# Performance work log

Hardware: AMD Instinct MI355X
Metric: run time of the kernel (lower is better)

The kernel has to match this reference:

```python
import jax, jax.numpy as jnp
import numpy as np

B, S, E, H = 2, 2048, 1024, 16
DH = E // H            # 64 head dim
ROT = DH // 2          # 32: RotaryEmbedding(head_dim//2) rotates first 32 dims only
CTX = 2048             # sliding KV window
THETA = 10000.0


def setup_inputs() -> dict:
    key = jax.random.key(0)
    ks = jax.random.split(key, 7)
    sc = 1.0 / np.sqrt(E)
    mk = lambda k, sh, s=1.0: (jax.random.normal(k, sh, jnp.float32) * s)
    return {
        "query": mk(ks[0], (B, S, E)),
        "key":   mk(ks[1], (B, S, E)),
        "value": mk(ks[2], (B, S, E)),
        "Wq": mk(ks[3], (E, E), sc), "bq": jnp.zeros((E,), jnp.float32),
        "Wk": mk(ks[4], (E, E), sc), "bk": jnp.zeros((E,), jnp.float32),
        "Wv": mk(ks[5], (E, E), sc), "bv": jnp.zeros((E,), jnp.float32),
        "Wo": mk(ks[6], (E, E), sc), "bo": jnp.zeros((E,), jnp.float32),
    }


def _rope(t):
    # t: [B, H, S, DH]; rotate first ROT dims, pass the rest through (offset=0).
    seq = t.shape[2]
    inv_freq = 1.0 / (THETA ** (jnp.arange(0, ROT, 2, dtype=jnp.float32) / ROT))  # [ROT//2]
    ang = jnp.arange(seq, dtype=jnp.float32)[:, None] * inv_freq[None, :]          # [S, ROT//2]
    cos = jnp.repeat(jnp.cos(ang), 2, axis=-1)  # [S, ROT] (pairwise-interleaved freqs)
    sin = jnp.repeat(jnp.sin(ang), 2, axis=-1)
    rot, rest = t[..., :ROT], t[..., ROT:]
    x1, x2 = rot[..., 0::2], rot[..., 1::2]
    rot_half = jnp.stack([-x2, x1], axis=-1).reshape(rot.shape)  # rotate_half on pairs
    return jnp.concatenate([rot * cos + rot_half * sin, rest], axis=-1)


def reference(query, key, value, Wq, bq, Wk, bk, Wv, bv, Wo, bo):
    def heads(x, W, b):
        return (x @ W.T + b).reshape(B, -1, H, DH).transpose(0, 2, 1, 3)  # [B,H,S,DH]

    q = _rope(heads(query, Wq, bq))
    k = _rope(heads(key, Wk, bk))
    v = heads(value, Wv, bv)
    k, v = k[:, :, -CTX:], v[:, :, -CTX:]  # sliding window (no-op when S == CTX)

    scale = jnp.float32(1.0 / np.sqrt(DH))
    scores = jnp.einsum('bhqd,bhkd->bhqk', q, k) * scale  # [B,H,Sq,Sk]
    sq, sk = q.shape[2], k.shape[2]
    causal = jnp.tril(jnp.ones((sk, sk), dtype=bool))[-sq:]  # [Sq,Sk]
    scores = jnp.where(causal[None, None], scores, jnp.float32(-jnp.inf))
    probs = jax.nn.softmax(scores, axis=-1)  # dropout=0 (eval)
    out = jnp.einsum('bhqk,bhkd->bhqd', probs, v)
    out = out.transpose(0, 2, 1, 3).reshape(B, -1, E)
    return out @ Wo.T + bo
```

## Files before the change

kernel.cpp:

```cpp
#include <hip/hip_runtime.h>
#include <stdint.h>
#include <math.h>

typedef __bf16 bf16x8 __attribute__((ext_vector_type(8)));
typedef float f32x4 __attribute__((ext_vector_type(4)));

__device__ __forceinline__ float bf2f(uint16_t x) {
  unsigned u = ((unsigned)x) << 16;
  float f;
  __builtin_memcpy(&f, &u, 4);
  return f;
}
__device__ __forceinline__ uint16_t f2bf(float f) {
  __bf16 h = (__bf16)f;
  uint16_t u;
  __builtin_memcpy(&u, &h, 2);
  return u;
}
__device__ __forceinline__ bf16x8 pack8(float4 lo, float4 hi) {
  bf16x8 v;
  v[0] = (__bf16)lo.x; v[1] = (__bf16)lo.y; v[2] = (__bf16)lo.z; v[3] = (__bf16)lo.w;
  v[4] = (__bf16)hi.x; v[5] = (__bf16)hi.y; v[6] = (__bf16)hi.z; v[7] = (__bf16)hi.w;
  return v;
}
__device__ __forceinline__ bf16x8 cvt8(const float* p) {
  return pack8(*(const float4*)p, *(const float4*)(p + 4));
}

typedef __attribute__((address_space(1))) const unsigned int gu32;
typedef __attribute__((address_space(3))) unsigned int lu32;
__device__ __forceinline__ void async_copy16(const void* gp, void* lp) {
  __builtin_amdgcn_global_load_lds((gu32*)gp, (lu32*)lp, 16, 0, 0);
}

__global__ __launch_bounds__(256) void cvt_kernel(
    const float* __restrict__ s0, uint16_t* __restrict__ d0,
    const float* __restrict__ s1, uint16_t* __restrict__ d1,
    const float* __restrict__ s2, uint16_t* __restrict__ d2,
    const float* __restrict__ s3, uint16_t* __restrict__ d3) {
  const int z = blockIdx.z;
  const float* s = z == 0 ? s0 : z == 1 ? s1 : z == 2 ? s2 : s3;
  uint16_t* d = z == 0 ? d0 : z == 1 ? d1 : z == 2 ? d2 : d3;
  const size_t idx = ((size_t)blockIdx.x * 256 + threadIdx.x) * 8;
  *(bf16x8*)(d + idx) = cvt8(s + idx);
}

template <bool A_F32, bool W_F32, bool C_F32, bool VT, bool ROPE, int BM, int NF>
__global__ __launch_bounds__(256) void gemm3_kernel(
    const void* __restrict__ A0, const void* __restrict__ W0,
    const float* __restrict__ b0, void* __restrict__ C0,
    const void* __restrict__ A1, const void* __restrict__ W1,
    const float* __restrict__ b1, void* __restrict__ C1,
    const void* __restrict__ A2, const void* __restrict__ W2,
    const float* __restrict__ b2, void* __restrict__ C2,
    int M, int N, int K) {
  constexpr int BN = NF * 32;
  constexpr int AF = BM / 32;
  const int z = blockIdx.z;
  const void* Av = z == 0 ? A0 : z == 1 ? A1 : A2;
  const void* Wp = z == 0 ? W0 : z == 1 ? W1 : W2;
  const float* bias = z == 0 ? b0 : z == 1 ? b1 : b2;
  void* Cv = z == 0 ? C0 : z == 1 ? C1 : C2;

  __shared__ __align__(16) uint16_t As[BM * 64];
  __shared__ __align__(16) uint16_t Bs[BN * 64];
  const int tid = threadIdx.x;
  const int wave = tid >> 6, lane = tid & 63;
  const int quad = lane >> 4, l16 = lane & 15;
  const int l = blockIdx.y * gridDim.x + blockIdx.x;
  const int nmt = M / BM;
  const int bm = (l % nmt) * BM;
  const int bn = (l / nmt) * BN;
  const int wm = (wave >> 1) * (BM / 2);
  const int wn = (wave & 1) * (BN / 2);

  f32x4 acc[AF][NF] = {};

  for (int k0 = 0; k0 < K; k0 += 64) {
    bf16x8 ar[AF], wr[NF];
    if (A_F32) {
#pragma unroll
      for (int i = 0; i < AF; i++) {
        const int c = i * 256 + tid;
        const int r = c >> 3, pc = ((c & 7) ^ (r & 7)) << 3;
        ar[i] = cvt8((const float*)Av + (size_t)(bm + r) * K + k0 + pc);
      }
    }
    if (W_F32) {
#pragma unroll
      for (int i = 0; i < NF; i++) {
        const int c = i * 256 + tid;
        const int r = c >> 3, pc = ((c & 7) ^ (r & 7)) << 3;
        wr[i] = cvt8((const float*)Wp + (size_t)(bn + r) * K + k0 + pc);
      }
    }
    if (k0) __syncthreads();
#pragma unroll
    for (int i = 0; i < AF; i++) {
      const int c = i * 256 + tid;
      const int r = c >> 3, pc = ((c & 7) ^ (r & 7)) << 3;
      if (A_F32) *(bf16x8*)(As + c * 8) = ar[i];
      else async_copy16((const uint16_t*)Av + (size_t)(bm + r) * K + k0 + pc,
                        As + (i * 256 + (tid & 192)) * 8);
    }
#pragma unroll
    for (int i = 0; i < NF; i++) {
      const int c = i * 256 + tid;
      const int r = c >> 3, pc = ((c & 7) ^ (r & 7)) << 3;
      if (W_F32) *(bf16x8*)(Bs + c * 8) = wr[i];
      else async_copy16((const uint16_t*)Wp + (size_t)(bn + r) * K + k0 + pc,
                        Bs + (i * 256 + (tid & 192)) * 8);
    }
    __syncthreads();
#pragma unroll
    for (int s = 0; s < 2; s++) {
      bf16x8 af[AF], bfr[NF];
#pragma unroll
      for (int i = 0; i < AF; i++) {
        const int Ra = wm + i * 16 + l16;
        af[i] = *(const bf16x8*)(As + Ra * 64 + (((s * 4 + quad) ^ (Ra & 7)) << 3));
      }
#pragma unroll
      for (int j = 0; j < NF; j++) {
        const int Rb = wn + j * 16 + l16;
        bfr[j] = *(const bf16x8*)(Bs + Rb * 64 + (((s * 4 + quad) ^ (Rb & 7)) << 3));
      }
#pragma unroll
      for (int i = 0; i < AF; i++)
#pragma unroll
        for (int j = 0; j < NF; j++)
          acc[i][j] = __builtin_amdgcn_mfma_f32_16x16x32_bf16(af[i], bfr[j], acc[i][j], 0, 0, 0);
    }
  }
  if (VT && z == 2) {
#pragma unroll
    for (int j = 0; j < NF; j++) {
      const int n = bn + wn + j * 16 + l16;
      const float bj = bias[n];
      const int h = n >> 6, dh = n & 63;
#pragma unroll
      for (int i = 0; i < AF; i++) {
        const int m0 = bm + wm + i * 16 + quad * 4;
        const int b = m0 >> 11, s0 = m0 & 2047;
        uint2 pk;
        pk.x = (unsigned)f2bf(acc[i][j][0] + bj) |
               ((unsigned)f2bf(acc[i][j][1] + bj) << 16);
        pk.y = (unsigned)f2bf(acc[i][j][2] + bj) |
               ((unsigned)f2bf(acc[i][j][3] + bj) << 16);
        *(uint2*)((uint16_t*)Cv + ((size_t)((b * 16 + h) * 64 + dh)) * 2048 + s0) = pk;
      }
    }
  } else {
#pragma unroll
    for (int j = 0; j < NF; j++) {
      const int n = bn + wn + j * 16 + l16;
      const float bj = bias[n];
      const int dh = (wn + j * 16 + l16) & 63;
      const bool rot = ROPE && (((wn + j * 16) & 63) < 32);
      float invrev = 0.f;
      if (rot)
        invrev = __expf(-0.5756462732485115f * (float)(dh >> 1)) *
                 0.15915494309189535f;
#pragma unroll
      for (int i = 0; i < AF; i++) {
        const int m0 = bm + wm + i * 16 + quad * 4;
#pragma unroll
        for (int r = 0; r < 4; r++) {
          float v = acc[i][j][r] + bj;
          if (rot) {
            const int s_pos = (m0 + r) & 2047;
            float rev = (float)s_pos * invrev;
            rev -= floorf(rev);
            const float sn = __builtin_amdgcn_sinf(rev);
            const float cs = __builtin_amdgcn_cosf(rev);
            const float partner = __shfl_xor(v, 1);
            v = (dh & 1) ? (v * cs + partner * sn) : (v * cs - partner * sn);
          }
          if (C_F32) ((float*)Cv)[(size_t)(m0 + r) * N + n] = v;
          else       ((uint16_t*)Cv)[(size_t)(m0 + r) * N + n] = f2bf(v);
        }
      }
    }
  }
}

__global__ __launch_bounds__(256) void flash_kernel(const uint16_t* __restrict__ Q,
                                                    const uint16_t* __restrict__ K,
                                                    const uint16_t* __restrict__ VT,
                                                    uint16_t* __restrict__ AO) {
  const int bx = blockIdx.x;
  const int xcd = bx & 7;
  const int slot = bx >> 3;
  const int bh = (slot >> 4) * 8 + xcd;
  const int qt2 = 15 - (slot & 15);
  const int h = bh & 15;
  const int b = bh >> 4;
  const int tid = threadIdx.x;
  const int wave = tid >> 6, lane = tid & 63;
  const int quad = lane >> 4, l16 = lane & 15;

  __shared__ __align__(16) uint16_t Ks[64 * 64];
  __shared__ __align__(16) uint16_t Vt[64 * 64];
  __shared__ __align__(16) uint16_t Ps[4][32 * 72];

  const int qrow0 = qt2 * 128 + wave * 16 + l16;
  const int qrow1 = qrow0 + 64;
  bf16x8 qf0[2], qf1[2];
#pragma unroll
  for (int s = 0; s < 2; s++) {
    union { bf16x8 v; uint16_t u[8]; } t0, t1;
    t0.v = *(const bf16x8*)(Q + ((size_t)(b * 2048 + qrow0) * 1024) + h * 64 + s * 32 + quad * 8);
    t1.v = *(const bf16x8*)(Q + ((size_t)(b * 2048 + qrow1) * 1024) + h * 64 + s * 32 + quad * 8);
#pragma unroll
    for (int j = 0; j < 8; j++) {
      t0.u[j] = f2bf(bf2f(t0.u[j]) * 0.125f);
      t1.u[j] = f2bf(bf2f(t1.u[j]) * 0.125f);
    }
    qf0[s] = t0.v;
    qf1[s] = t1.v;
  }

  const size_t vbase = ((size_t)((b * 16 + h) * 64)) * 2048;

  float lsum0 = 0.f, lsum1 = 0.f;
  f32x4 o0[4] = {}, o1[4] = {};

  const int nkt = 2 * qt2 + 2;
  for (int kt = 0; kt < nkt; kt++) {
    if (kt) __syncthreads();
#pragma unroll
    for (int i = 0; i < 2; i++) {
      const int c = i * 256 + tid;
      const int r = c >> 3, pc = ((c & 7) ^ (r & 7)) << 3;
      async_copy16(K + ((size_t)(b * 2048 + kt * 64 + r) * 1024) + h * 64 + pc,
                   Ks + (i * 256 + (tid & 192)) * 8);
      async_copy16(VT + vbase + (size_t)r * 2048 + kt * 64 + pc,
                   Vt + (i * 256 + (tid & 192)) * 8);
    }
    __syncthreads();

    const bool f0 = (kt < nkt - 1);

    {
      f32x4 sacc[4] = {};
#pragma unroll
      for (int s = 0; s < 2; s++)
#pragma unroll
        for (int t = 0; t < 4; t++) {
          const int R = t * 16 + l16;
          bf16x8 kf = *(const bf16x8*)(Ks + R * 64 + (((s * 4 + quad) ^ (R & 7)) << 3));
          sacc[t] = __builtin_amdgcn_mfma_f32_16x16x32_bf16(kf, qf1[s], sacc[t], 0, 0, 0);
        }
      if (kt == nkt - 1) {
#pragma unroll
        for (int t = 0; t < 4; t++)
#pragma unroll
          for (int r = 0; r < 4; r++)
            if (kt * 64 + t * 16 + quad * 4 + r > qrow1) sacc[t][r] = -1e30f;
      }
#pragma unroll
      for (int t = 0; t < 4; t++) {
        float p0 = __expf(sacc[t][0]), p1 = __expf(sacc[t][1]);
        float p2 = __expf(sacc[t][2]), p3 = __expf(sacc[t][3]);
        lsum1 += (p0 + p1) + (p2 + p3);
        uint2 pk;
        pk.x = (unsigned)f2bf(p0) | ((unsigned)f2bf(p1) << 16);
        pk.y = (unsigned)f2bf(p2) | ((unsigned)f2bf(p3) << 16);
        *(uint2*)(&Ps[wave][(16 + l16) * 72 + t * 16 + quad * 4]) = pk;
      }
    }
    if (f0) {
      f32x4 sacc[4] = {};
#pragma unroll
      for (int s = 0; s < 2; s++)
#pragma unroll
        for (int t = 0; t < 4; t++) {
          const int R = t * 16 + l16;
          bf16x8 kf = *(const bf16x8*)(Ks + R * 64 + (((s * 4 + quad) ^ (R & 7)) << 3));
          sacc[t] = __builtin_amdgcn_mfma_f32_16x16x32_bf16(kf, qf0[s], sacc[t], 0, 0, 0);
        }
      if (kt == nkt - 2) {
#pragma unroll
        for (int t = 0; t < 4; t++)
#pragma unroll
          for (int r = 0; r < 4; r++)
            if (kt * 64 + t * 16 + quad * 4 + r > qrow0) sacc[t][r] = -1e30f;
      }
#pragma unroll
      for (int t = 0; t < 4; t++) {
        float p0 = __expf(sacc[t][0]), p1 = __expf(sacc[t][1]);
        float p2 = __expf(sacc[t][2]), p3 = __expf(sacc[t][3]);
        lsum0 += (p0 + p1) + (p2 + p3);
        uint2 pk;
        pk.x = (unsigned)f2bf(p0) | ((unsigned)f2bf(p1) << 16);
        pk.y = (unsigned)f2bf(p2) | ((unsigned)f2bf(p3) << 16);
        *(uint2*)(&Ps[wave][l16 * 72 + t * 16 + quad * 4]) = pk;
      }
    }
#pragma unroll
    for (int s = 0; s < 2; s++) {
      const bf16x8 pa1 = *(const bf16x8*)(&Ps[wave][(16 + l16) * 72 + s * 32 + quad * 8]);
#pragma unroll
      for (int t = 0; t < 4; t++) {
        const int R = t * 16 + l16;
        const bf16x8 vb = *(const bf16x8*)(Vt + R * 64 + (((s * 4 + quad) ^ (R & 7)) << 3));
        o1[t] = __builtin_amdgcn_mfma_f32_16x16x32_bf16(pa1, vb, o1[t], 0, 0, 0);
      }
    }
    if (f0) {
#pragma unroll
      for (int s = 0; s < 2; s++) {
        const bf16x8 pa0 = *(const bf16x8*)(&Ps[wave][l16 * 72 + s * 32 + quad * 8]);
#pragma unroll
        for (int t = 0; t < 4; t++) {
          const int R = t * 16 + l16;
          const bf16x8 vb = *(const bf16x8*)(Vt + R * 64 + (((s * 4 + quad) ^ (R & 7)) << 3));
          o0[t] = __builtin_amdgcn_mfma_f32_16x16x32_bf16(pa0, vb, o0[t], 0, 0, 0);
        }
      }
    }
  }
  lsum0 += __shfl_xor(lsum0, 16);
  lsum0 += __shfl_xor(lsum0, 32);
  lsum1 += __shfl_xor(lsum1, 16);
  lsum1 += __shfl_xor(lsum1, 32);
  const float inv0 = 1.f / lsum0, inv1 = 1.f / lsum1;
  float invr0[4], invr1[4];
#pragma unroll
  for (int r = 0; r < 4; r++) {
    invr0[r] = __shfl(inv0, quad * 4 + r);
    invr1[r] = __shfl(inv1, quad * 4 + r);
  }
#pragma unroll
  for (int t = 0; t < 4; t++)
#pragma unroll
    for (int r = 0; r < 4; r++) {
      const int qg0 = qt2 * 128 + wave * 16 + quad * 4 + r;
      AO[((size_t)(b * 2048 + qg0) * 1024) + h * 64 + t * 16 + l16] =
          f2bf(o0[t][r] * invr0[r]);
      AO[((size_t)(b * 2048 + qg0 + 64) * 1024) + h * 64 + t * 16 + l16] =
          f2bf(o1[t][r] * invr1[r]);
    }
}

extern "C" void kernel_launch(void* const* d_in, const int* in_sizes, int n_in,
                              void* d_out, int out_size, void* d_ws, size_t ws_size,
                              hipStream_t stream) {
  const float* query = (const float*)d_in[0];
  const float* key   = (const float*)d_in[1];
  const float* value = (const float*)d_in[2];
  const float* Wq = (const float*)d_in[3];
  const float* bq = (const float*)d_in[4];
  const float* Wk = (const float*)d_in[5];
  const float* bk = (const float*)d_in[6];
  const float* Wv = (const float*)d_in[7];
  const float* bv = (const float*)d_in[8];
  const float* Wo = (const float*)d_in[9];
  const float* bo = (const float*)d_in[10];
  float* out = (float*)d_out;

  uint16_t* ws = (uint16_t*)d_ws;
  uint16_t* Qb  = ws;
  uint16_t* Kb  = ws + (size_t)4194304;
  uint16_t* VTb = ws + (size_t)8388608;
  uint16_t* AOb = ws + (size_t)12582912;

  dim3 blk(256);

  if (ws_size >= (size_t)64 * 1024 * 1024) {
    uint16_t* Qc  = ws + (size_t)16777216;
    uint16_t* Kc  = ws + (size_t)20971520;
    uint16_t* Vc  = ws + (size_t)25165824;
    uint16_t* Wqc = ws + (size_t)29360128;
    uint16_t* Wkc = ws + (size_t)30408704;
    uint16_t* Wvc = ws + (size_t)31457280;
    uint16_t* Woc = ws + (size_t)32505856;

    cvt_kernel<<<dim3(512, 1, 4), blk, 0, stream>>>(
        Wq, Wqc, Wk, Wkc, Wv, Wvc, Wo, Woc);
    cvt_kernel<<<dim3(2048, 1, 3), blk, 0, stream>>>(
        query, Qc, key, Kc, value, Vc, nullptr, nullptr);
    gemm3_kernel<false, false, false, true, true, 128, 4><<<dim3(8, 32, 3), blk, 0, stream>>>(
        Qc, Wqc, bq, Qb,
        Kc, Wkc, bk, Kb,
        Vc, Wvc, bv, VTb,
        4096, 1024, 1024);
    flash_kernel<<<dim3(512), blk, 0, stream>>>(Qb, Kb, VTb, AOb);
    gemm3_kernel<false, false, true, false, false, 128, 2><<<dim3(16, 32, 1), blk, 0, stream>>>(
        AOb, Woc, bo, out,
        AOb, Woc, bo, out,
        AOb, Woc, bo, out,
        4096, 1024, 1024);
  } else {
    uint16_t* Wqc = AOb;
    uint16_t* Wkc = AOb + (size_t)1048576;
    uint16_t* Wvc = AOb + (size_t)2097152;
    cvt_kernel<<<dim3(512, 1, 3), blk, 0, stream>>>(
        Wq, Wqc, Wk, Wkc, Wv, Wvc, nullptr, nullptr);
    gemm3_kernel<true, false, false, true, true, 128, 2><<<dim3(16, 32, 3), blk, 0, stream>>>(
        query, Wqc, bq, Qb,
        key,   Wkc, bk, Kb,
        value, Wvc, bv, VTb,
        4096, 1024, 1024);
    flash_kernel<<<dim3(512), blk, 0, stream>>>(Qb, Kb, VTb, AOb);
    gemm3_kernel<false, true, true, false, false, 128, 2><<<dim3(16, 32, 1), blk, 0, stream>>>(
        AOb, Wo, bo, out,
        AOb, Wo, bo, out,
        AOb, Wo, bo, out,
        4096, 1024, 1024);
  }
}
```

Before: 230.0 us.

## Split flash attention blocks to one 64-row query tile each

Each flash-attention block now handles a single 64-row query tile instead of two 64-row tiles per 128-row chunk, doubling the grid to 1024 blocks. Each block streams K/V tiles only up to its own causal limit. This uses more workgroups and fewer registers per block, which should raise occupancy and balance the causal work better. The cost is that every K/V tile is loaded from global memory twice as often, because the K/V reuse between the two query tiles is lost.

```diff
diff --git a/kernel.cpp b/kernel.cpp
--- a/kernel.cpp
+++ b/kernel.cpp
@@ -191,8 +191,8 @@
   const int bx = blockIdx.x;
   const int xcd = bx & 7;
   const int slot = bx >> 3;
-  const int bh = (slot >> 4) * 8 + xcd;
-  const int qt2 = 15 - (slot & 15);
+  const int bh = (slot >> 5) * 8 + xcd;
+  const int qt = 31 - (slot & 31);
   const int h = bh & 15;
   const int b = bh >> 4;
   const int tid = threadIdx.x;
@@ -201,31 +201,25 @@
 
   __shared__ __align__(16) uint16_t Ks[64 * 64];
   __shared__ __align__(16) uint16_t Vt[64 * 64];
-  __shared__ __align__(16) uint16_t Ps[4][32 * 72];
-
-  const int qrow0 = qt2 * 128 + wave * 16 + l16;
-  const int qrow1 = qrow0 + 64;
-  bf16x8 qf0[2], qf1[2];
+  __shared__ __align__(16) uint16_t Ps[4][16 * 72];
+
+  const int qrow = qt * 64 + wave * 16 + l16;
+  bf16x8 qf[2];
 #pragma unroll
   for (int s = 0; s < 2; s++) {
-    union { bf16x8 v; uint16_t u[8]; } t0, t1;
-    t0.v = *(const bf16x8*)(Q + ((size_t)(b * 2048 + qrow0) * 1024) + h * 64 + s * 32 + quad * 8);
-    t1.v = *(const bf16x8*)(Q + ((size_t)(b * 2048 + qrow1) * 1024) + h * 64 + s * 32 + quad * 8);
-#pragma unroll
-    for (int j = 0; j < 8; j++) {
-      t0.u[j] = f2bf(bf2f(t0.u[j]) * 0.125f);
-      t1.u[j] = f2bf(bf2f(t1.u[j]) * 0.125f);
-    }
-    qf0[s] = t0.v;
-    qf1[s] = t1.v;
+    union { bf16x8 v; uint16_t u[8]; } t0;
+    t0.v = *(const bf16x8*)(Q + ((size_t)(b * 2048 + qrow) * 1024) + h * 64 + s * 32 + quad * 8);
+#pragma unroll
+    for (int j = 0; j < 8; j++) t0.u[j] = f2bf(bf2f(t0.u[j]) * 0.125f);
+    qf[s] = t0.v;
   }
 
   const size_t vbase = ((size_t)((b * 16 + h) * 64)) * 2048;
 
-  float lsum0 = 0.f, lsum1 = 0.f;
-  f32x4 o0[4] = {}, o1[4] = {};
-
-  const int nkt = 2 * qt2 + 2;
+  float lsum = 0.f;
+  f32x4 o[4] = {};
+
+  const int nkt = qt + 1;
   for (int kt = 0; kt < nkt; kt++) {
     if (kt) __syncthreads();
 #pragma unroll
@@ -239,107 +233,56 @@
     }
     __syncthreads();
 
-    const bool f0 = (kt < nkt - 1);
-
-    {
-      f32x4 sacc[4] = {};
-#pragma unroll
-      for (int s = 0; s < 2; s++)
-#pragma unroll
-        for (int t = 0; t < 4; t++) {
-          const int R = t * 16 + l16;
-          bf16x8 kf = *(const bf16x8*)(Ks + R * 64 + (((s * 4 + quad) ^ (R & 7)) << 3));
-          sacc[t] = __builtin_amdgcn_mfma_f32_16x16x32_bf16(kf, qf1[s], sacc[t], 0, 0, 0);
-        }
-      if (kt == nkt - 1) {
-#pragma unroll
-        for (int t = 0; t < 4; t++)
-#pragma unroll
-          for (int r = 0; r < 4; r++)
-            if (kt * 64 + t * 16 + quad * 4 + r > qrow1) sacc[t][r] = -1e30f;
-      }
+    f32x4 sacc[4] = {};
+#pragma unroll
+    for (int s = 0; s < 2; s++)
 #pragma unroll
       for (int t = 0; t < 4; t++) {
-        float p0 = __expf(sacc[t][0]), p1 = __expf(sacc[t][1]);
-        float p2 = __expf(sacc[t][2]), p3 = __expf(sacc[t][3]);
-        lsum1 += (p0 + p1) + (p2 + p3);
-        uint2 pk;
-        pk.x = (unsigned)f2bf(p0) | ((unsigned)f2bf(p1) << 16);
-        pk.y = (unsigned)f2bf(p2) | ((unsigned)f2bf(p3) << 16);
-        *(uint2*)(&Ps[wave][(16 + l16) * 72 + t * 16 + quad * 4]) = pk;
-      }
-    }
-    if (f0) {
-      f32x4 sacc[4] = {};
-#pragma unroll
-      for (int s = 0; s < 2; s++)
-#pragma unroll
-        for (int t = 0; t < 4; t++) {
-          const int R = t * 16 + l16;
-          bf16x8 kf = *(const bf16x8*)(Ks + R * 64 + (((s * 4 + quad) ^ (R & 7)) << 3));
-          sacc[t] = __builtin_amdgcn_mfma_f32_16x16x32_bf16(kf, qf0[s], sacc[t], 0, 0, 0);
-        }
-      if (kt == nkt - 2) {
-#pragma unroll
-        for (int t = 0; t < 4; t++)
-#pragma unroll
-          for (int r = 0; r < 4; r++)
-            if (kt * 64 + t * 16 + quad * 4 + r > qrow0) sacc[t][r] = -1e30f;
-      }
-#pragma unroll
-      for (int t = 0; t < 4; t++) {
-        float p0 = __expf(sacc[t][0]), p1 = __expf(sacc[t][1]);
-        float p2 = __expf(sacc[t][2]), p3 = __expf(sacc[t][3]);
-        lsum0 += (p0 + p1) + (p2 + p3);
-        uint2 pk;
-        pk.x = (unsigned)f2bf(p0) | ((unsigned)f2bf(p1) << 16);
-        pk.y = (unsigned)f2bf(p2) | ((unsigned)f2bf(p3) << 16);
-        *(uint2*)(&Ps[wave][l16 * 72 + t * 16 + quad * 4]) = pk;
-      }
+        const int R = t * 16 + l16;
+        bf16x8 kf = *(const bf16x8*)(Ks + R * 64 + (((s * 4 + quad) ^ (R & 7)) << 3));
+        sacc[t] = __builtin_amdgcn_mfma_f32_16x16x32_bf16(kf, qf[s], sacc[t], 0, 0, 0);
+      }
+    if (kt == qt) {
+#pragma unroll
+      for (int t = 0; t < 4; t++)
+#pragma unroll
+        for (int r = 0; r < 4; r++)
+          if (kt * 64 + t * 16 + quad * 4 + r > qrow) sacc[t][r] = -1e30f;
+    }
+#pragma unroll
+    for (int t = 0; t < 4; t++) {
+      float p0 = __expf(sacc[t][0]), p1 = __expf(sacc[t][1]);
+      float p2 = __expf(sacc[t][2]), p3 = __expf(sacc[t][3]);
+      lsum += (p0 + p1) + (p2 + p3);
+      uint2 pk;
+      pk.x = (unsigned)f2bf(p0) | ((unsigned)f2bf(p1) << 16);
+      pk.y = (unsigned)f2bf(p2) | ((unsigned)f2bf(p3) << 16);
+      *(uint2*)(&Ps[wave][l16 * 72 + t * 16 + quad * 4]) = pk;
     }
 #pragma unroll
     for (int s = 0; s < 2; s++) {
-      const bf16x8 pa1 = *(const bf16x8*)(&Ps[wave][(16 + l16) * 72 + s * 32 + quad * 8]);
+      const bf16x8 pa = *(const bf16x8*)(&Ps[wave][l16 * 72 + s * 32 + quad * 8]);
 #pragma unroll
       for (int t = 0; t < 4; t++) {
         const int R = t * 16 + l16;
         const bf16x8 vb = *(const bf16x8*)(Vt + R * 64 + (((s * 4 + quad) ^ (R & 7)) << 3));
-        o1[t] = __builtin_amdgcn_mfma_f32_16x16x32_bf16(pa1, vb, o1[t], 0, 0, 0);
-      }
-    }
-    if (f0) {
-#pragma unroll
-      for (int s = 0; s < 2; s++) {
-        const bf16x8 pa0 = *(const bf16x8*)(&Ps[wave][l16 * 72 + s * 32 + quad * 8]);
-#pragma unroll
-        for (int t = 0; t < 4; t++) {
-          const int R = t * 16 + l16;
-          const bf16x8 vb = *(const bf16x8*)(Vt + R * 64 + (((s * 4 + quad) ^ (R & 7)) << 3));
-          o0[t] = __builtin_amdgcn_mfma_f32_16x16x32_bf16(pa0, vb, o0[t], 0, 0, 0);
-        }
-      }
-    }
-  }
-  lsum0 += __shfl_xor(lsum0, 16);
-  lsum0 += __shfl_xor(lsum0, 32);
-  lsum1 += __shfl_xor(lsum1, 16);
-  lsum1 += __shfl_xor(lsum1, 32);
-  const float inv0 = 1.f / lsum0, inv1 = 1.f / lsum1;
-  float invr0[4], invr1[4];
-#pragma unroll
-  for (int r = 0; r < 4; r++) {
-    invr0[r] = __shfl(inv0, quad * 4 + r);
-    invr1[r] = __shfl(inv1, quad * 4 + r);
-  }
+        o[t] = __builtin_amdgcn_mfma_f32_16x16x32_bf16(pa, vb, o[t], 0, 0, 0);
+      }
+    }
+  }
+  lsum += __shfl_xor(lsum, 16);
+  lsum += __shfl_xor(lsum, 32);
+  const float inv = 1.f / lsum;
+  float invr[4];
+#pragma unroll
+  for (int r = 0; r < 4; r++) invr[r] = __shfl(inv, quad * 4 + r);
 #pragma unroll
   for (int t = 0; t < 4; t++)
 #pragma unroll
     for (int r = 0; r < 4; r++) {
-      const int qg0 = qt2 * 128 + wave * 16 + quad * 4 + r;
-      AO[((size_t)(b * 2048 + qg0) * 1024) + h * 64 + t * 16 + l16] =
-          f2bf(o0[t][r] * invr0[r]);
-      AO[((size_t)(b * 2048 + qg0 + 64) * 1024) + h * 64 + t * 16 + l16] =
-          f2bf(o1[t][r] * invr1[r]);
+      const int qg = qt * 64 + wave * 16 + quad * 4 + r;
+      AO[((size_t)(b * 2048 + qg) * 1024) + h * 64 + t * 16 + l16] =
+          f2bf(o[t][r] * invr[r]);
     }
 }
 
@@ -385,7 +328,7 @@
         Kc, Wkc, bk, Kb,
         Vc, Wvc, bv, VTb,
         4096, 1024, 1024);
-    flash_kernel<<<dim3(512), blk, 0, stream>>>(Qb, Kb, VTb, AOb);
+    flash_kernel<<<dim3(1024), blk, 0, stream>>>(Qb, Kb, VTb, AOb);
     gemm3_kernel<false, false, true, false, false, 128, 2><<<dim3(16, 32, 1), blk, 0, stream>>>(
         AOb, Woc, bo, out,
         AOb, Woc, bo, out,
@@ -402,7 +345,7 @@
         key,   Wkc, bk, Kb,
         value, Wvc, bv, VTb,
         4096, 1024, 1024);
-    flash_kernel<<<dim3(512), blk, 0, stream>>>(Qb, Kb, VTb, AOb);
+    flash_kernel<<<dim3(1024), blk, 0, stream>>>(Qb, Kb, VTb, AOb);
     gemm3_kernel<false, true, true, false, false, 128, 2><<<dim3(16, 32, 1), blk, 0, stream>>>(
         AOb, Wo, bo, out,
         AOb, Wo, bo, out,
```

After: 229.8 us. No clear change (-0.1%).

## Load K and V fragments directly from global memory, dropping shared-memory staging

Applied to the files above, without the earlier changes.

The flash attention loop no longer stages K and V tiles through LDS with async copies and block barriers. Each wave now loads its K and V^T MFMA fragments straight from global memory into registers and reuses each fragment for both query row groups. This removes the two __syncthreads per tile and the LDS traffic. In exchange, all four waves fetch the same K/V data redundantly from global/L2, with strided 16-byte accesses and no prefetch overlap.

```diff
diff --git a/kernel.cpp b/kernel.cpp
--- a/kernel.cpp
+++ b/kernel.cpp
@@ -199,8 +199,6 @@
   const int wave = tid >> 6, lane = tid & 63;
   const int quad = lane >> 4, l16 = lane & 15;
 
-  __shared__ __align__(16) uint16_t Ks[64 * 64];
-  __shared__ __align__(16) uint16_t Vt[64 * 64];
   __shared__ __align__(16) uint16_t Ps[4][32 * 72];
 
   const int qrow0 = qt2 * 128 + wave * 16 + l16;
@@ -220,76 +218,61 @@
     qf1[s] = t1.v;
   }
 
-  const size_t vbase = ((size_t)((b * 16 + h) * 64)) * 2048;
+  const uint16_t* Kh = K + (size_t)(b * 2048) * 1024 + h * 64;
+  const uint16_t* Vh = VT + ((size_t)((b * 16 + h) * 64)) * 2048;
 
   float lsum0 = 0.f, lsum1 = 0.f;
   f32x4 o0[4] = {}, o1[4] = {};
 
   const int nkt = 2 * qt2 + 2;
   for (int kt = 0; kt < nkt; kt++) {
-    if (kt) __syncthreads();
-#pragma unroll
-    for (int i = 0; i < 2; i++) {
-      const int c = i * 256 + tid;
-      const int r = c >> 3, pc = ((c & 7) ^ (r & 7)) << 3;
-      async_copy16(K + ((size_t)(b * 2048 + kt * 64 + r) * 1024) + h * 64 + pc,
-                   Ks + (i * 256 + (tid & 192)) * 8);
-      async_copy16(VT + vbase + (size_t)r * 2048 + kt * 64 + pc,
-                   Vt + (i * 256 + (tid & 192)) * 8);
-    }
-    __syncthreads();
-
     const bool f0 = (kt < nkt - 1);
 
-    {
-      f32x4 sacc[4] = {};
-#pragma unroll
-      for (int s = 0; s < 2; s++)
-#pragma unroll
-        for (int t = 0; t < 4; t++) {
-          const int R = t * 16 + l16;
-          bf16x8 kf = *(const bf16x8*)(Ks + R * 64 + (((s * 4 + quad) ^ (R & 7)) << 3));
-          sacc[t] = __builtin_amdgcn_mfma_f32_16x16x32_bf16(kf, qf1[s], sacc[t], 0, 0, 0);
-        }
-      if (kt == nkt - 1) {
+    f32x4 sacc1[4] = {}, sacc0[4] = {};
+#pragma unroll
+    for (int s = 0; s < 2; s++) {
+      bf16x8 kf[4];
+#pragma unroll
+      for (int t = 0; t < 4; t++)
+        kf[t] = *(const bf16x8*)(Kh + (size_t)(kt * 64 + t * 16 + l16) * 1024 + s * 32 + quad * 8);
+#pragma unroll
+      for (int t = 0; t < 4; t++)
+        sacc1[t] = __builtin_amdgcn_mfma_f32_16x16x32_bf16(kf[t], qf1[s], sacc1[t], 0, 0, 0);
+      if (f0) {
 #pragma unroll
         for (int t = 0; t < 4; t++)
+          sacc0[t] = __builtin_amdgcn_mfma_f32_16x16x32_bf16(kf[t], qf0[s], sacc0[t], 0, 0, 0);
+      }
+    }
+    if (kt == nkt - 1) {
+#pragma unroll
+      for (int t = 0; t < 4; t++)
+#pragma unroll
+        for (int r = 0; r < 4; r++)
+          if (kt * 64 + t * 16 + quad * 4 + r > qrow1) sacc1[t][r] = -1e30f;
+    }
+#pragma unroll
+    for (int t = 0; t < 4; t++) {
+      float p0 = __expf(sacc1[t][0]), p1 = __expf(sacc1[t][1]);
+      float p2 = __expf(sacc1[t][2]), p3 = __expf(sacc1[t][3]);
+      lsum1 += (p0 + p1) + (p2 + p3);
+      uint2 pk;
+      pk.x = (unsigned)f2bf(p0) | ((unsigned)f2bf(p1) << 16);
+      pk.y = (unsigned)f2bf(p2) | ((unsigned)f2bf(p3) << 16);
+      *(uint2*)(&Ps[wave][(16 + l16) * 72 + t * 16 + quad * 4]) = pk;
+    }
+    if (f0) {
+      if (kt == nkt - 2) {
+#pragma unroll
+        for (int t = 0; t < 4; t++)
 #pragma unroll
           for (int r = 0; r < 4; r++)
-            if (kt * 64 + t * 16 + quad * 4 + r > qrow1) sacc[t][r] = -1e30f;
+            if (kt * 64 + t * 16 + quad * 4 + r > qrow0) sacc0[t][r] = -1e30f;
       }
 #pragma unroll
       for (int t = 0; t < 4; t++) {
-        float p0 = __expf(sacc[t][0]), p1 = __expf(sacc[t][1]);
-        float p2 = __expf(sacc[t][2]), p3 = __expf(sacc[t][3]);
-        lsum1 += (p0 + p1) + (p2 + p3);
-        uint2 pk;
-        pk.x = (unsigned)f2bf(p0) | ((unsigned)f2bf(p1) << 16);
-        pk.y = (unsigned)f2bf(p2) | ((unsigned)f2bf(p3) << 16);
-        *(uint2*)(&Ps[wave][(16 + l16) * 72 + t * 16 + quad * 4]) = pk;
-      }
-    }
-    if (f0) {
-      f32x4 sacc[4] = {};
-#pragma unroll
-      for (int s = 0; s < 2; s++)
-#pragma unroll
-        for (int t = 0; t < 4; t++) {
-          const int R = t * 16 + l16;
-          bf16x8 kf = *(const bf16x8*)(Ks + R * 64 + (((s * 4 + quad) ^ (R & 7)) << 3));
-          sacc[t] = __builtin_amdgcn_mfma_f32_16x16x32_bf16(kf, qf0[s], sacc[t], 0, 0, 0);
-        }
-      if (kt == nkt - 2) {
-#pragma unroll
-        for (int t = 0; t < 4; t++)
-#pragma unroll
-          for (int r = 0; r < 4; r++)
-            if (kt * 64 + t * 16 + quad * 4 + r > qrow0) sacc[t][r] = -1e30f;
-      }
-#pragma unroll
-      for (int t = 0; t < 4; t++) {
-        float p0 = __expf(sacc[t][0]), p1 = __expf(sacc[t][1]);
-        float p2 = __expf(sacc[t][2]), p3 = __expf(sacc[t][3]);
+        float p0 = __expf(sacc0[t][0]), p1 = __expf(sacc0[t][1]);
+        float p2 = __expf(sacc0[t][2]), p3 = __expf(sacc0[t][3]);
         lsum0 += (p0 + p1) + (p2 + p3);
         uint2 pk;
         pk.x = (unsigned)f2bf(p0) | ((unsigned)f2bf(p1) << 16);
@@ -299,24 +282,19 @@
     }
 #pragma unroll
     for (int s = 0; s < 2; s++) {
+      bf16x8 vb[4];
+#pragma unroll
+      for (int t = 0; t < 4; t++)
+        vb[t] = *(const bf16x8*)(Vh + (size_t)(t * 16 + l16) * 2048 + kt * 64 + s * 32 + quad * 8);
       const bf16x8 pa1 = *(const bf16x8*)(&Ps[wave][(16 + l16) * 72 + s * 32 + quad * 8]);
 #pragma unroll
-      for (int t = 0; t < 4; t++) {
-        const int R = t * 16 + l16;
-        const bf16x8 vb = *(const bf16x8*)(Vt + R * 64 + (((s * 4 + quad) ^ (R & 7)) << 3));
-        o1[t] = __builtin_amdgcn_mfma_f32_16x16x32_bf16(pa1, vb, o1[t], 0, 0, 0);
-      }
-    }
-    if (f0) {
-#pragma unroll
-      for (int s = 0; s < 2; s++) {
+      for (int t = 0; t < 4; t++)
+        o1[t] = __builtin_amdgcn_mfma_f32_16x16x32_bf16(pa1, vb[t], o1[t], 0, 0, 0);
+      if (f0) {
         const bf16x8 pa0 = *(const bf16x8*)(&Ps[wave][l16 * 72 + s * 32 + quad * 8]);
 #pragma unroll
-        for (int t = 0; t < 4; t++) {
-          const int R = t * 16 + l16;
-          const bf16x8 vb = *(const bf16x8*)(Vt + R * 64 + (((s * 4 + quad) ^ (R & 7)) << 3));
-          o0[t] = __builtin_amdgcn_mfma_f32_16x16x32_bf16(pa0, vb, o0[t], 0, 0, 0);
-        }
+        for (int t = 0; t < 4; t++)
+          o0[t] = __builtin_amdgcn_mfma_f32_16x16x32_bf16(pa0, vb[t], o0[t], 0, 0, 0);
       }
     }
   }
```

After: 288.5 us. 25.4% more time.
